# Performance work log

Measured on AMD Instinct MI355X. Metric: run time of the kernel, lower is better.

Reference implementation:

```python
import jax, jax.numpy as jnp
from jax import lax
import numpy as np

N, M, P, K = 2, 16384, 5023, 4
C_PLANE, HP = 32, 256
OUT_DIM = 32


def _harmonic(x):
    # pytorch3d HarmonicEmbedding(n=4, logspace, omega_0=1, append_input=True)
    f = jnp.asarray([1.0, 2.0, 4.0, 8.0], x.dtype)
    e = (x[..., None] * f).reshape(x.shape[:-1] + (-1,))  # [..., 12]
    return jnp.concatenate([jnp.sin(e), jnp.cos(e), x], axis=-1)  # [..., 27]


def _grid_sample2d(img, grid):
    # img [C,H,W], grid [M,2] (x->W, y->H) in [-1,1]; bilinear, zero pad, align_corners=False
    C, H, W = img.shape
    x = (grid[:, 0] + 1.0) * (W / 2.0) - 0.5
    y = (grid[:, 1] + 1.0) * (H / 2.0) - 0.5
    x0 = jnp.floor(x); y0 = jnp.floor(y)
    x1 = x0 + 1.0; y1 = y0 + 1.0
    wx1 = x - x0; wx0 = 1.0 - wx1
    wy1 = y - y0; wy0 = 1.0 - wy1
    def gather(ix, iy):
        valid = ((ix >= 0) & (ix < W) & (iy >= 0) & (iy < H)).astype(img.dtype)
        ixc = jnp.clip(ix, 0, W - 1).astype(jnp.int32)
        iyc = jnp.clip(iy, 0, H - 1).astype(jnp.int32)
        return img[:, iyc, ixc] * valid[None, :]  # [C,M]
    out = (gather(x0, y0) * (wx0 * wy0) + gather(x1, y0) * (wx1 * wy0)
           + gather(x0, y1) * (wx0 * wy1) + gather(x1, y1) * (wx1 * wy1))
    return out.T  # [M,C]


def _forward(coordinates, directions, points_position, tex_tplanes, emb_table,
             pw1, pb1, pw2, pb2, fw1, fb1, fw2, fb2, fw3, fb3, dw, db, rw1, rb1, rw2, rb2):
    c = coordinates
    p = points_position
    # --- triplane sampling (EG3D projections (x,y),(x,z),(z,x)), mean over planes ---
    proj = jnp.stack([c[..., :2],
                      c[..., jnp.array([0, 2])],
                      c[..., jnp.array([2, 0])]], axis=1)  # [N,3,M,2]
    tex = jax.vmap(jax.vmap(_grid_sample2d))(tex_tplanes, proj).mean(axis=1)  # [N,M,32]
    # --- KNN (squared distances, ascending, as pytorch3d knn_points) ---
    d2 = (jnp.sum(c * c, -1)[:, :, None] + jnp.sum(p * p, -1)[:, None, :]
          - 2.0 * jnp.einsum('nmc,npc->nmp', c, p))  # [N,M,P]
    negd, idx = lax.top_k(-d2, K)
    dist = -negd  # [N,M,K]
    nn = jax.vmap(lambda pts, i: pts[i])(p, idx)  # [N,M,K,3]
    pf = emb_table[idx]  # [N,M,K,32]
    rel = c[:, :, None, :] - nn
    rel = rel / jnp.maximum(jnp.linalg.norm(rel, axis=-1, keepdims=True), 1e-12)
    h = jnp.concatenate([pf, _harmonic(rel)], axis=-1)  # [N,M,K,59]
    h = jax.nn.relu(h @ pw1 + pb1) @ pw2 + pb2  # [N,M,K,32]
    w = 1.0 / dist
    w = w / jnp.sum(w, axis=1, keepdims=True)  # dim=1 exactly as in source
    pts_feat = jnp.sum(h * w[..., None], axis=2)  # [N,M,32]
    # --- dense MLP stack ---
    feat = jnp.concatenate([tex, pts_feat], axis=-1)  # [N,M,64]
    feat = jax.nn.relu(feat @ fw1 + fb1)
    feat = jax.nn.relu(feat @ fw2 + fb2)
    feat = feat @ fw3 + fb3  # [N,M,128]
    selector = jnp.all((c > -1.0) & (c < 1.0), axis=-1)  # [N,M]
    raw = (jax.nn.softplus(10.0 * (feat @ dw + db)) / 10.0) * selector[..., None]
    densities = 1.0 - jnp.exp(-raw)
    rays = directions / jnp.maximum(jnp.linalg.norm(directions, axis=-1, keepdims=True), 1e-12)
    rgb = jnp.concatenate([feat, _harmonic(rays)], axis=-1)  # [N,M,155]
    rgb = jax.nn.relu(rgb @ rw1 + rb1) @ rw2 + rb2  # [N,M,OUT_DIM]
    rgb = jnp.concatenate([jax.nn.sigmoid(rgb[..., :3]) * (1.0 + 2 * 0.001) - 0.001,
                           rgb[..., 3:]], axis=-1)
    return densities, rgb, dist


def setup_inputs() -> dict:
    key = jax.random.key(0)
    ks = jax.random.split(key, 16)
    rn = lambda k, s, sc=1.0: jax.random.normal(k, s, jnp.float32) * sc
    def lin(k, i, o):
        k1, k2 = jax.random.split(k)
        return rn(k1, (i, o), 1.0 / np.sqrt(i)), rn(k2, (o,), 0.01)
    coordinates = jax.random.uniform(ks[0], (N, M, 3), jnp.float32)
    directions = rn(ks[1], (N, M, 3))
    points_position = jax.random.uniform(ks[2], (N, P, 3), jnp.float32)
    tex_tplanes = rn(ks[3], (N, 3, C_PLANE, HP, HP))
    emb_table = rn(ks[4], (P, 32), 0.02)
    pw1, pb1 = lin(ks[5], 32 + 27, 64)
    pw2, pb2 = lin(ks[6], 64, 32)
    fw1, fb1 = lin(ks[7], 64, 128)
    fw2, fb2 = lin(ks[8], 128, 128)
    fw3, fb3 = lin(ks[9], 128, 128)
    dw, db = lin(ks[10], 128, 1)
    rw1, rb1 = lin(ks[11], 128 + 27, 64)
    rw2, rb2 = lin(ks[12], 64, OUT_DIM)
    return dict(coordinates=coordinates, directions=directions, points_position=points_position,
                tex_tplanes=tex_tplanes, emb_table=emb_table, pw1=pw1, pb1=pb1, pw2=pw2, pb2=pb2,
                fw1=fw1, fb1=fb1, fw2=fw2, fb2=fb2, fw3=fw3, fb3=fb3, dw=dw, db=db,
                rw1=rw1, rb1=rb1, rw2=rw2, rb2=rb2)


def reference(coordinates, directions, points_position, tex_tplanes, emb_table,
              pw1, pb1, pw2, pb2, fw1, fb1, fw2, fb2, fw3, fb3, dw, db, rw1, rb1, rw2, rb2):
    return _forward(coordinates, directions, points_position, tex_tplanes, emb_table,
                    pw1, pb1, pw2, pb2, fw1, fb1, fw2, fb2, fw3, fb3, dw, db, rw1, rb1, rw2, rb2)
```

## Files before the change

kernel.cpp:

```cpp
#include <hip/hip_runtime.h>
#include <float.h>
#include <math.h>

#define NB 2
#define MQ 16384
#define NQ (NB*MQ)
#define PP 5023
#define KNN 4
#define HPX 256
#define HWSZ (HPX*HPX)
#define GD 12
#define GC (GD*GD*GD)
#define CAND_MAX 1024

#define OUT_RGB_OFF  ((size_t)NQ)
#define OUT_DIST_OFF ((size_t)NQ + (size_t)NQ*32)

#define WS_SUMS_OFF   ((size_t)0x80000)
#define WS_PCNT_OFF   ((size_t)0x81000)
#define WS_PSTART_OFF ((size_t)0x85000)
#define WS_PCUR_OFF   ((size_t)0x89000)
#define WS_QCNT_OFF   ((size_t)0x8D000)
#define WS_QSTART_OFF ((size_t)0x91000)
#define WS_QCUR_OFF   ((size_t)0x95000)
// ... 168 lines not shown
    const int gz = c / (GD*GD), gy = (c / GD) % GD, gx = c % GD;

    const int x0 = max(gx-2,0), x1 = min(gx+2,GD-1);
    const int y0 = max(gy-2,0), y1 = min(gy+2,GD-1), ny = y1-y0+1;
    const int z0 = max(gz-2,0), z1 = min(gz+2,GD-1), nz = z1-z0+1;
    const int nrow = ny*nz;

    __shared__ unsigned int rcnt[25];
    if (tid < nrow) {
        const int yy = y0 + tid % ny;
        const int zz = z0 + tid / ny;
        const int c0 = n*GC + (zz*GD + yy)*GD + x0;
        const int c1 = n*GC + (zz*GD + yy)*GD + x1;
        const unsigned int s = pstart[c0];
        rs[tid]   = s;
        rcnt[tid] = (pstart[c1] + pcnt[c1]) - s;
    }
    __syncthreads();
    if (tid == 0) {
        unsigned int acc = 0; ro[0] = 0;
        for (int t = 0; t < nrow; ++t) { acc += rcnt[t]; ro[t+1] = acc; }
    }
    __syncthreads();
    const unsigned int total = ro[nrow];
    const bool ovf = (total > CAND_MAX);
    if (!ovf) {
        for (unsigned int i = tid; i < total; i += 256) {
            int lo = 0, hi = nrow;
            while (hi - lo > 1) { int mid = (lo + hi) >> 1; if (ro[mid] <= i) lo = mid; else hi = mid; }
            const unsigned int src = rs[lo] + (i - ro[lo]);
            cand[i] = pg[src];
            cidx[i] = pid[src];
        }
    }
    __syncthreads();

    const float w = 1.0f / (float)GD;
    const float thresh = 4.f * w * w * 0.999f;
    const int grp = tid >> 4, l16 = tid & 15;
    const unsigned int qs = qstart[n*GC + c];

#define INS4(d, i) { \
        bool L3 = ((d) < bd3) || ((d) == bd3 && (i) < bi3); \
        bool L2 = ((d) < bd2) || ((d) == bd2 && (i) < bi2); \
        bool L1 = ((d) < bd1) || ((d) == bd1 && (i) < bi1); \
        bool L0 = ((d) < bd0) || ((d) == bd0 && (i) < bi0); \
        bd3 = L3 ? (L2 ? bd2 : (d)) : bd3;  bi3 = L3 ? (L2 ? bi2 : (i)) : bi3; \
        bd2 = L2 ? (L1 ? bd1 : (d)) : bd2;  bi2 = L2 ? (L1 ? bi1 : (i)) : bi2; \
        bd1 = L1 ? (L0 ? bd0 : (d)) : bd1;  bi1 = L1 ? (L0 ? bi0 : (i)) : bi1; \
        bd0 = L0 ? (d) : bd0;               bi0 = L0 ? (i) : bi0; }

#define MERGE16() { \
        float bd[4] = { bd0, bd1, bd2, bd3 }; \
        int   bi[4] = { bi0, bi1, bi2, bi3 }; \
        for (int mask = 1; mask < 16; mask <<= 1) { \
            float od[4]; int oi[4]; \
            for (int j = 0; j < 4; ++j) { od[j] = __shfl_xor(bd[j], mask); \
                                          oi[j] = __shfl_xor(bi[j], mask); } \
            float e[4]; int ei[4]; \
            for (int j = 0; j < 4; ++j) { \
                float ad = bd[j], xd = od[3-j]; \
                int   ai = bi[j], xi = oi[3-j]; \
                bool ta = (ad < xd) || (ad == xd && ai < xi); \
                e[j] = ta ? ad : xd; ei[j] = ta ? ai : xi; \
            } \
            { bool sw = (e[2] < e[0]) || (e[2] == e[0] && ei[2] < ei[0]); \
              if (sw) { float td=e[0]; e[0]=e[2]; e[2]=td; int ti=ei[0]; ei[0]=ei[2]; ei[2]=ti; } } \
            { bool sw = (e[3] < e[1]) || (e[3] == e[1] && ei[3] < ei[1]); \
              if (sw) { float td=e[1]; e[1]=e[3]; e[3]=td; int ti=ei[1]; ei[1]=ei[3]; ei[3]=ti; } } \
            { bool sw = (e[1] < e[0]) || (e[1] == e[0] && ei[1] < ei[0]); \
              if (sw) { float td=e[0]; e[0]=e[1]; e[1]=td; int ti=ei[0]; ei[0]=ei[1]; ei[1]=ti; } } \
            { bool sw = (e[3] < e[2]) || (e[3] == e[2] && ei[3] < ei[2]); \
              if (sw) { float td=e[2]; e[2]=e[3]; e[3]=td; int ti=ei[2]; ei[2]=ei[3]; ei[3]=ti; } } \
            for (int j = 0; j < 4; ++j) { bd[j] = e[j]; bi[j] = ei[j]; } \
        } \
        bd0 = bd[0]; bd1 = bd[1]; bd2 = bd[2]; bd3 = bd[3]; \
        bi0 = bi[0]; bi1 = bi[1]; bi2 = bi[2]; bi3 = bi[3]; }

#pragma unroll 1
    for (unsigned int qb = 0; qb < qn; qb += 16) {
        const unsigned int qi = qb + grp;
        if (qi >= qn) continue;
        const int q = qid[qs + qi];
        const float cx = coords[3*q], cy = coords[3*q+1], cz = coords[3*q+2];
        const float ccq = fmaf(cx, cx, fmaf(cy, cy, cz*cz));

        float bd0 = FLT_MAX, bd1 = FLT_MAX, bd2 = FLT_MAX, bd3 = FLT_MAX;
        int   bi0 = 0x7fffffff, bi1 = 0x7fffffff, bi2 = 0x7fffffff, bi3 = 0x7fffffff;

        if (!ovf) {
#pragma unroll 1
            for (unsigned int j = l16; j < total; j += 16) {
                const float4 P = cand[j];
                const int i = cidx[j];
                const float dt = fmaf(cx, P.x, fmaf(cy, P.y, cz * P.z));
                const float d = fmaf(-2.0f, dt, ccq + P.w);
                INS4(d, i)
            }
            MERGE16()
        }
        if (ovf || !(bd3 < thresh)) {
            bd0 = bd1 = bd2 = bd3 = FLT_MAX;
            bi0 = bi1 = bi2 = bi3 = 0x7fffffff;
#pragma unroll 1
            for (int j = l16; j < PP; j += 16) {
                const float4 P = pg[n*PP + j];
                const int i = pid[n*PP + j];
                const float dt = fmaf(cx, P.x, fmaf(cy, P.y, cz * P.z));
                const float d = fmaf(-2.0f, dt, ccq + P.w);
                INS4(d, i)
            }
            MERGE16()
        }
        if (l16 == 0) {
            *(float4*)(odist + (size_t)q*4) = make_float4(bd0, bd1, bd2, bd3);
            *(int4*)(oidx + (size_t)q*4)    = make_int4(bi0, bi1, bi2, bi3);
        }
    }
#undef INS4
#undef MERGE16
}

__global__ __launch_bounds__(1024) void k_sums(const float* __restrict__ dist,
                                               float* __restrict__ sums) {
    const int b = blockIdx.x;
    const int n = b >> 2, k = b & 3;
    float s = 0.f;
    for (int m = threadIdx.x; m < MQ; m += 1024)
        s += 1.0f / dist[((size_t)n * MQ + m) * 4 + k];
    __shared__ float red[1024];
    red[threadIdx.x] = s;
    __syncthreads();
    for (int off = 512; off > 0; off >>= 1) {
        if (threadIdx.x < off) red[threadIdx.x] += red[threadIdx.x + off];
        __syncthreads();
    }
    if (threadIdx.x == 0) sums[b] = red[0];
}

static __device__ __forceinline__ float harm_val(int h, float rx, float ry, float rz) {
    if (h >= 27) return 0.f;
    float v;
    if (h < 24) {
        int base = (h < 12) ? h : (h - 12);
        float rv = (base >> 2) == 0 ? rx : ((base >> 2) == 1 ? ry : rz);
        float e = rv * (float)(1 << (base & 3));
        v = (h < 12) ? sinf(e) : cosf(e);
    } else {
        v = (h == 24) ? rx : ((h == 25) ? ry : rz);
    }
    return v;
}

#define SW 128

template<int DIN2, int DOUT, int TILE>
__device__ __forceinline__ void gemv2(const unsigned int* Xp, int lane,
                                      const unsigned int* Wl,
                                      const float* __restrict__ bias, int j0,
                                      float (&aa)[TILE], float (&ab)[TILE]) {
    static_assert(TILE % 4 == 0, "");
#pragma unroll
    for (int u = 0; u < TILE; ++u) { aa[u] = bias[j0 + u]; ab[u] = aa[u]; }
#pragma unroll
    for (int i2 = 0; i2 < DIN2; ++i2) {
        const uint2 xv = *(const uint2*)(Xp + i2 * SW + 2*lane);
        const uint4* wr = (const uint4*)(Wl + i2 * DOUT + j0);
#pragma unroll
        for (int t = 0; t < TILE/4; ++t) {
            const uint4 w4 = wr[t];
            aa[4*t+0] = dot2(xv.x, w4.x, aa[4*t+0]);  ab[4*t+0] = dot2(xv.y, w4.x, ab[4*t+0]);
            aa[4*t+1] = dot2(xv.x, w4.y, aa[4*t+1]);  ab[4*t+1] = dot2(xv.y, w4.y, ab[4*t+1]);
            aa[4*t+2] = dot2(xv.x, w4.z, aa[4*t+2]);  ab[4*t+2] = dot2(xv.y, w4.z, ab[4*t+2]);
            aa[4*t+3] = dot2(xv.x, w4.w, aa[4*t+3]);  ab[4*t+3] = dot2(xv.y, w4.w, ab[4*t+3]);
        }
    }
}

__global__ __launch_bounds__(1024, 1) void k_main(
    const float* __restrict__ coords, const float* __restrict__ dirs,
    const float* __restrict__ pts, const float* __restrict__ tex_raw,
    const unsigned int* __restrict__ tex16, const float* __restrict__ emb,
    const unsigned int* __restrict__ wp,
    const float* __restrict__ pb1, const float* __restrict__ pb2,
    const float* __restrict__ fb1, const float* __restrict__ fb2,
    const float* __restrict__ fb3, const float* __restrict__ db,
    const float* __restrict__ rb1, const float* __restrict__ rb2,
    const int* __restrict__ idxbuf, const float* __restrict__ distbuf,
    const float* __restrict__ sums, float* __restrict__ out, int use_tex_t)
{
    __shared__ unsigned int S[128 * SW];
    __shared__ __align__(16) unsigned int W[8192];
    const int tid  = threadIdx.x;
    const int lane = tid & 63;
    const int wv   = __builtin_amdgcn_readfirstlane(tid >> 6);
    const int q0   = blockIdx.x * 128;
    const int n    = q0 >> 14;
    const int qa   = q0 + 2*lane, qb = qa + 1;

#define STAGE(dstu4, srcoff, len) { \
        const uint4* s4_ = (const uint4*)(wp + (srcoff)); \
        for (int i_ = tid; i_ < (len)/4; i_ += 1024) ((uint4*)W)[(dstu4) + i_] = s4_[i_]; }

    unsigned int tex_pack[2];
    {
        const int g = wv;
#pragma unroll
        for (int s = 0; s < 2; ++s) {
            const int q = qa + s;
            const float cx = coords[q*3+0], cy = coords[q*3+1], cz = coords[q*3+2];
            float a0 = 0.f, a1 = 0.f;
#pragma unroll
            for (int pl = 0; pl < 3; ++pl) {
                float gx = (pl == 2) ? cz : cx;
                float gy = (pl == 0) ? cy : ((pl == 1) ? cz : cx);
                float x = (gx + 1.f) * 128.f - 0.5f;
                float y = (gy + 1.f) * 128.f - 0.5f;
                float x0f = floorf(x), y0f = floorf(y);
                float wx1 = x - x0f, wy1 = y - y0f;
                float wx0 = 1.f - wx1, wy0 = 1.f - wy1;
                int x0 = (int)x0f, y0 = (int)y0f;
                int n3 = n * 3 + pl;
                int  xs[4] = { x0, x0+1, x0,   x0+1 };
                int  ys[4] = { y0, y0,   y0+1, y0+1 };
                float wt[4] = { wx0*wy0, wx1*wy0, wx0*wy1, wx1*wy1 };
#pragma unroll
                for (int c = 0; c < 4; ++c) {
                    int xi = xs[c], yi = ys[c];
                    if (xi >= 0 && xi < HPX && yi >= 0 && yi < HPX) {
                        float wgt = wt[c];
                        if (use_tex_t) {
                            const unsigned int v = tex16[
                                ((size_t)n3 * HWSZ + (size_t)yi * HPX + xi) * 16 + g];
                            const float2 f = upk(v);
                            a0 = fmaf(wgt, f.x, a0);
                            a1 = fmaf(wgt, f.y, a1);
                        } else {
                            size_t base = ((size_t)(n3 * 32 + g * 2)) * HWSZ + (size_t)yi * HPX + xi;
                            a0 = fmaf(wgt, tex_raw[base], a0);
                            a1 = fmaf(wgt, tex_raw[base + HWSZ], a1);
                        }
                    }
                }
            }
            tex_pack[s] = pk2(a0 * (1.f/3.f), a1 * (1.f/3.f));
        }
    }

    STAGE(0, WP_PW1, 1920)
    STAGE(512, WP_PW2, 1024)
    __syncthreads();

#pragma unroll 1
    for (int k = 0; k < KNN; ++k) {
        {
#pragma unroll
            for (int s = 0; s < 2; ++s) {
                const int q = qa + s;
                const int id = idxbuf[(size_t)q*4 + k];
                if (wv < 8) {
                    const float4 e = *(const float4*)(emb + (size_t)id * 32 + wv*4);
                    S[(64 + 2*wv    )*SW + 2*lane + s] = pk2(e.x, e.y);
                    S[(64 + 2*wv + 1)*SW + 2*lane + s] = pk2(e.z, e.w);
                } else {
                    const int w8 = wv - 8;
                    if (w8 < 7) {
                        const float cx = coords[q*3+0], cy = coords[q*3+1], cz = coords[q*3+2];
                        const float nx = pts[((size_t)n*PP + id)*3 + 0];
                        const float ny = pts[((size_t)n*PP + id)*3 + 1];
                        const float nz = pts[((size_t)n*PP + id)*3 + 2];
                        float rx = cx - nx, ry = cy - ny, rz = cz - nz;
                        float nrm = sqrtf(fmaf(rx, rx, fmaf(ry, ry, rz*rz)));
                        float inv = 1.f / fmaxf(nrm, 1e-12f);
                        rx *= inv; ry *= inv; rz *= inv;
#pragma unroll
                        for (int t = 0; t < 2; ++t) {
                            const int pr = 2*w8 + t;
                            S[(80 + pr)*SW + 2*lane + s] =
                                pk2(harm_val(2*pr, rx, ry, rz), harm_val(2*pr + 1, rx, ry, rz));
                        }
                    }
                }
            }
        }
        __syncthreads();
        {
            float aa[4], ab[4];
            gemv2<30, 64, 4>(S + 64*SW, lane, W, pb1, wv * 4, aa, ab);
            S[(96 + 2*wv    )*SW + 2*lane + 0] = pk2(fmaxf(aa[0], 0.f), fmaxf(aa[1], 0.f));
            S[(96 + 2*wv    )*SW + 2*lane + 1] = pk2(fmaxf(ab[0], 0.f), fmaxf(ab[1], 0.f));
            S[(96 + 2*wv + 1)*SW + 2*lane + 0] = pk2(fmaxf(aa[2], 0.f), fmaxf(aa[3], 0.f));
            S[(96 + 2*wv + 1)*SW + 2*lane + 1] = pk2(fmaxf(ab[2], 0.f), fmaxf(ab[3], 0.f));
        }
        __syncthreads();
        {
            float aa[2], ab[2];
            aa[0] = pb2[wv*2 + 0]; aa[1] = pb2[wv*2 + 1];
            ab[0] = aa[0]; ab[1] = aa[1];
#pragma unroll
            for (int i2 = 0; i2 < 32; ++i2) {
                const uint2 xv = *(const uint2*)(S + (96 + i2)*SW + 2*lane);
                const unsigned int w0 = W[2048 + i2*32 + wv*2 + 0];
                const unsigned int w1 = W[2048 + i2*32 + wv*2 + 1];
                aa[0] = dot2(xv.x, w0, aa[0]);  ab[0] = dot2(xv.y, w0, ab[0]);
                aa[1] = dot2(xv.x, w1, aa[1]);  ab[1] = dot2(xv.y, w1, ab[1]);
            }
            const float da = distbuf[(size_t)qa*4 + k];
            const float dbq = distbuf[(size_t)qb*4 + k];
            const float wka = (1.0f / da)  / sums[n*4 + k];
            const float wkb = (1.0f / dbq) / sums[n*4 + k];
            S[(k*16 + wv)*SW + 2*lane + 0] = pk2(wka * aa[0], wka * aa[1]);
            S[(k*16 + wv)*SW + 2*lane + 1] = pk2(wkb * ab[0], wkb * ab[1]);
        }
        __syncthreads();
    }

    {
        S[(64 + wv)*SW + 2*lane + 0] = tex_pack[0];
        S[(64 + wv)*SW + 2*lane + 1] = tex_pack[1];
#pragma unroll
        for (int s = 0; s < 2; ++s) {
            float a = 0.f, b = 0.f;
#pragma unroll
            for (int k = 0; k < 4; ++k) {
                float2 v = upk(S[(k*16 + wv)*SW + 2*lane + s]);
                a += v.x; b += v.y;
            }
            S[(80 + wv)*SW + 2*lane + s] = pk2(a, b);
        }
    }
    STAGE(0, WP_FW1, 4096)
    __syncthreads();
    {
        float aa[8], ab[8];
        gemv2<32, 128, 8>(S + 64*SW, lane, W, fb1, wv * 8, aa, ab);
#pragma unroll
        for (int u = 0; u < 4; ++u) {
            S[(4*wv + u)*SW + 2*lane + 0] = pk2(fmaxf(aa[2*u], 0.f), fmaxf(aa[2*u+1], 0.f));
            S[(4*wv + u)*SW + 2*lane + 1] = pk2(fmaxf(ab[2*u], 0.f), fmaxf(ab[2*u+1], 0.f));
        }
    }
    __syncthreads();
    STAGE(0, WP_FW2, 8192)
    __syncthreads();
    {
        float aa[8], ab[8];
        gemv2<64, 128, 8>(S, lane, W, fb2, wv * 8, aa, ab);
#pragma unroll
        for (int u = 0; u < 4; ++u) {
            S[(64 + 4*wv + u)*SW + 2*lane + 0] = pk2(fmaxf(aa[2*u], 0.f), fmaxf(aa[2*u+1], 0.f));
            S[(64 + 4*wv + u)*SW + 2*lane + 1] = pk2(fmaxf(ab[2*u], 0.f), fmaxf(ab[2*u+1], 0.f));
        }
    }
    __syncthreads();
    STAGE(0, WP_FW3, 8192)
    __syncthreads();
    {
        float aa[8], ab[8];
        gemv2<64, 128, 8>(S + 64*SW, lane, W, fb3, wv * 8, aa, ab);
#pragma unroll
        for (int u = 0; u < 4; ++u) {
            S[(4*wv + u)*SW + 2*lane + 0] = pk2(aa[2*u], aa[2*u+1]);
            S[(4*wv + u)*SW + 2*lane + 1] = pk2(ab[2*u], ab[2*u+1]);
        }
    }
    __syncthreads();
    STAGE(0, WP_RW1, 4992)
    STAGE(1248, WP_RW2, 1024)
    STAGE(1504, WP_DW, 64)
    if (wv < 14) {
#pragma unroll
        for (int s = 0; s < 2; ++s) {
            const int q = qa + s;
            float dx = dirs[q*3+0], dy = dirs[q*3+1], dz = dirs[q*3+2];
            float dn = sqrtf(fmaf(dx, dx, fmaf(dy, dy, dz*dz)));
            float inv = 1.f / fmaxf(dn, 1e-12f);
            dx *= inv; dy *= inv; dz *= inv;
            S[(64 + wv)*SW + 2*lane + s] = pk2(harm_val(2*wv, dx, dy, dz),
                                               harm_val(2*wv + 1, dx, dy, dz));
        }
    }
    __syncthreads();
    {
        float aa[4], ab[4];
        gemv2<78, 64, 4>(S, lane, W, rb1, wv * 4, aa, ab);
        S[(78 + 2*wv    )*SW + 2*lane + 0] = pk2(fmaxf(aa[0], 0.f), fmaxf(aa[1], 0.f));
        S[(78 + 2*wv    )*SW + 2*lane + 1] = pk2(fmaxf(ab[0], 0.f), fmaxf(ab[1], 0.f));
        S[(78 + 2*wv + 1)*SW + 2*lane + 0] = pk2(fmaxf(aa[2], 0.f), fmaxf(aa[3], 0.f));
        S[(78 + 2*wv + 1)*SW + 2*lane + 1] = pk2(fmaxf(ab[2], 0.f), fmaxf(ab[3], 0.f));
    }
    __syncthreads();
    {
        float aa[2], ab[2];
        aa[0] = rb2[wv*2 + 0]; aa[1] = rb2[wv*2 + 1];
        ab[0] = aa[0]; ab[1] = aa[1];
#pragma unroll
        for (int i2 = 0; i2 < 32; ++i2) {
            const uint2 xv = *(const uint2*)(S + (78 + i2)*SW + 2*lane);
            const unsigned int w0 = W[4992 + i2*32 + wv*2 + 0];
            const unsigned int w1 = W[4992 + i2*32 + wv*2 + 1];
            aa[0] = dot2(xv.x, w0, aa[0]);  ab[0] = dot2(xv.y, w0, ab[0]);
            aa[1] = dot2(xv.x, w1, aa[1]);  ab[1] = dot2(xv.y, w1, ab[1]);
        }
#pragma unroll
        for (int u = 0; u < 2; ++u) {
            const int j = wv*2 + u;
            float va = (u == 0) ? aa[0] : aa[1];
            float vb = (u == 0) ? ab[0] : ab[1];
            if (j < 3) {
                va = 1.002f * (1.f / (1.f + expf(-va))) - 0.001f;
                vb = 1.002f * (1.f / (1.f + expf(-vb))) - 0.001f;
            }
            out[OUT_RGB_OFF + (size_t)qa*32 + j] = va;
            out[OUT_RGB_OFF + (size_t)qb*32 + j] = vb;
        }
        if (wv == 15) {
            float za = db[0], zb = db[0];
#pragma unroll 1
            for (int i2 = 0; i2 < 64; ++i2) {
                const uint2 xv = *(const uint2*)(S + i2*SW + 2*lane);
                const unsigned int wz = W[6016 + i2];
                za = dot2(xv.x, wz, za);
                zb = dot2(xv.y, wz, zb);
            }
#pragma unroll
            for (int s = 0; s < 2; ++s) {
                const int q = qa + s;
                const float z = (s == 0) ? za : zb;
                const float cx = coords[q*3+0], cy = coords[q*3+1], cz = coords[q*3+2];
                float selv = (cx > -1.f && cx < 1.f && cy > -1.f && cy < 1.f &&
                              cz > -1.f && cz < 1.f) ? 1.f : 0.f;
                float t10 = 10.f * z;
                float sp = (t10 > 20.f) ? t10 : log1pf(expf(t10));
                float raw = sp * 0.1f * selv;
                out[q] = 1.f - expf(-raw);
            }
        }
    }
#undef STAGE
}

extern "C" void kernel_launch(void* const* d_in, const int* in_sizes, int n_in,
                              void* d_out, int out_size, void* d_ws, size_t ws_size,
                              hipStream_t stream) {
    (void)in_sizes; (void)n_in; (void)out_size;
    const float* coords = (const float*)d_in[0];
    const float* dirs   = (const float*)d_in[1];
    const float* pts    = (const float*)d_in[2];
    const float* tex    = (const float*)d_in[3];
    const float* emb    = (const float*)d_in[4];
    const float* pw1 = (const float*)d_in[5];  const float* pb1 = (const float*)d_in[6];
    const float* pw2 = (const float*)d_in[7];  const float* pb2 = (const float*)d_in[8];
    const float* fw1 = (const float*)d_in[9];  const float* fb1 = (const float*)d_in[10];
    const float* fw2 = (const float*)d_in[11]; const float* fb2 = (const float*)d_in[12];
    const float* fw3 = (const float*)d_in[13]; const float* fb3 = (const float*)d_in[14];
    const float* dw  = (const float*)d_in[15]; const float* db  = (const float*)d_in[16];
    const float* rw1 = (const float*)d_in[17]; const float* rb1 = (const float*)d_in[18];
    const float* rw2 = (const float*)d_in[19]; const float* rb2 = (const float*)d_in[20];

    float*        out     = (float*)d_out;
    int*          wsidx   = (int*)d_ws;
    float*        wssums  = (float*)((char*)d_ws + WS_SUMS_OFF);
    unsigned int* wspcnt  = (unsigned int*)((char*)d_ws + WS_PCNT_OFF);
    unsigned int* wspsta  = (unsigned int*)((char*)d_ws + WS_PSTART_OFF);
    unsigned int* wspcur  = (unsigned int*)((char*)d_ws + WS_PCUR_OFF);
    unsigned int* wsqcnt  = (unsigned int*)((char*)d_ws + WS_QCNT_OFF);
    unsigned int* wsqsta  = (unsigned int*)((char*)d_ws + WS_QSTART_OFF);
    unsigned int* wsqcur  = (unsigned int*)((char*)d_ws + WS_QCUR_OFF);
    int*          wsqid   = (int*)((char*)d_ws + WS_QID_OFF);
    float4*       wspg    = (float4*)((char*)d_ws + WS_PG_OFF);
    int*          wspid   = (int*)((char*)d_ws + WS_PID_OFF);
    unsigned int* wswp    = (unsigned int*)((char*)d_ws + WS_WP_OFF);
    unsigned int* wstex   = (unsigned int*)((char*)d_ws + WS_TEX_OFF);

    const size_t need_tex = WS_TEX_OFF + (size_t)6 * HWSZ * 16 * 4;
    const int use_t = (ws_size >= need_tex) ? 1 : 0;

    PackArgs pa;
    pa.src[0] = pw1; pa.off[0] = WP_PW1; pa.din[0] = 59;  pa.dout[0] = 64;
    pa.src[1] = pw2; pa.off[1] = WP_PW2; pa.din[1] = 64;  pa.dout[1] = 32;
    pa.src[2] = fw1; pa.off[2] = WP_FW1; pa.din[2] = 64;  pa.dout[2] = 128;
    pa.src[3] = fw2; pa.off[3] = WP_FW2; pa.din[3] = 128; pa.dout[3] = 128;
    pa.src[4] = fw3; pa.off[4] = WP_FW3; pa.din[4] = 128; pa.dout[4] = 128;
    pa.src[5] = dw;  pa.off[5] = WP_DW;  pa.din[5] = 128; pa.dout[5] = 1;
    pa.src[6] = rw1; pa.off[6] = WP_RW1; pa.din[6] = 155; pa.dout[6] = 64;
    pa.src[7] = rw2; pa.off[7] = WP_RW2; pa.din[7] = 64;  pa.dout[7] = 32;

    const int nitems = NB*PP + NQ;
    hipMemsetAsync((char*)d_ws + WS_PCNT_OFF, 0, WS_QSTART_OFF - WS_PCNT_OFF, stream);
    k_pack<<<dim3(32, 8), 256, 0, stream>>>(pa, wswp);
    if (use_t) k_transpose<<<6 * 256, 256, 0, stream>>>(tex, wstex);
    k_count<<<(nitems + 255)/256, 256, 0, stream>>>(pts, coords, wspcnt, wsqcnt);
    k_scan2<<<1, 1024, 0, stream>>>(wspcnt, wspsta, wspcur, wsqcnt, wsqsta, wsqcur);
    k_scatter<<<(nitems + 255)/256, 256, 0, stream>>>(pts, coords, wspcur, wsqcur,
                                                      wspg, wspid, wsqid);
    k_knn_cell<<<NB*GC, 256, 0, stream>>>(coords, wspsta, wspcnt, wspg, wspid,
                                          wsqsta, wsqcnt, wsqid,
                                          out + OUT_DIST_OFF, wsidx);
    k_sums<<<8, 1024, 0, stream>>>(out + OUT_DIST_OFF, wssums);
    k_main<<<NQ / 128, 1024, 0, stream>>>(coords, dirs, pts, tex, wstex, emb,
                                          wswp, pb1, pb2, fb1, fb2, fb3, db, rb1, rb2,
                                          wsidx, out + OUT_DIST_OFF, wssums, out, use_t);
}
```

Baseline: 280.2 us.

## Process one query per lane in the main MLP kernel to raise occupancy

```diff
diff --git a/kernel.cpp b/kernel.cpp
--- a/kernel.cpp
+++ b/kernel.cpp
@@ -344,32 +344,32 @@
     return v;
 }
 
-#define SW 128
+#define SW 64
 
 template<int DIN2, int DOUT, int TILE>
-__device__ __forceinline__ void gemv2(const unsigned int* Xp, int lane,
+__device__ __forceinline__ void gemv1(const unsigned int* Xp, int lane,
                                       const unsigned int* Wl,
                                       const float* __restrict__ bias, int j0,
-                                      float (&aa)[TILE], float (&ab)[TILE]) {
+                                      float (&aa)[TILE]) {
     static_assert(TILE % 4 == 0, "");
 #pragma unroll
-    for (int u = 0; u < TILE; ++u) { aa[u] = bias[j0 + u]; ab[u] = aa[u]; }
+    for (int u = 0; u < TILE; ++u) aa[u] = bias[j0 + u];
 #pragma unroll
     for (int i2 = 0; i2 < DIN2; ++i2) {
-        const uint2 xv = *(const uint2*)(Xp + i2 * SW + 2*lane);
+        const unsigned int xv = Xp[i2 * SW + lane];
         const uint4* wr = (const uint4*)(Wl + i2 * DOUT + j0);
 #pragma unroll
         for (int t = 0; t < TILE/4; ++t) {
             const uint4 w4 = wr[t];
-            aa[4*t+0] = dot2(xv.x, w4.x, aa[4*t+0]);  ab[4*t+0] = dot2(xv.y, w4.x, ab[4*t+0]);
-            aa[4*t+1] = dot2(xv.x, w4.y, aa[4*t+1]);  ab[4*t+1] = dot2(xv.y, w4.y, ab[4*t+1]);
-            aa[4*t+2] = dot2(xv.x, w4.z, aa[4*t+2]);  ab[4*t+2] = dot2(xv.y, w4.z, ab[4*t+2]);
-            aa[4*t+3] = dot2(xv.x, w4.w, aa[4*t+3]);  ab[4*t+3] = dot2(xv.y, w4.w, ab[4*t+3]);
-        }
-    }
-}
-
-__global__ __launch_bounds__(1024, 1) void k_main(
+            aa[4*t+0] = dot2(xv, w4.x, aa[4*t+0]);
+            aa[4*t+1] = dot2(xv, w4.y, aa[4*t+1]);
+            aa[4*t+2] = dot2(xv, w4.z, aa[4*t+2]);
+            aa[4*t+3] = dot2(xv, w4.w, aa[4*t+3]);
+        }
+    }
+}
+
+__global__ __launch_bounds__(1024, 8) void k_main(
     const float* __restrict__ coords, const float* __restrict__ dirs,
     const float* __restrict__ pts, const float* __restrict__ tex_raw,
     const unsigned int* __restrict__ tex16, const float* __restrict__ emb,
@@ -386,57 +386,54 @@
     const int tid  = threadIdx.x;
     const int lane = tid & 63;
     const int wv   = __builtin_amdgcn_readfirstlane(tid >> 6);
-    const int q0   = blockIdx.x * 128;
+    const int q0   = blockIdx.x * 64;
     const int n    = q0 >> 14;
-    const int qa   = q0 + 2*lane, qb = qa + 1;
+    const int qa   = q0 + lane;
 
 #define STAGE(dstu4, srcoff, len) { \
         const uint4* s4_ = (const uint4*)(wp + (srcoff)); \
         for (int i_ = tid; i_ < (len)/4; i_ += 1024) ((uint4*)W)[(dstu4) + i_] = s4_[i_]; }
 
-    unsigned int tex_pack[2];
+    unsigned int tex_pack;
     {
         const int g = wv;
-#pragma unroll
-        for (int s = 0; s < 2; ++s) {
-            const int q = qa + s;
-            const float cx = coords[q*3+0], cy = coords[q*3+1], cz = coords[q*3+2];
-            float a0 = 0.f, a1 = 0.f;
-#pragma unroll
-            for (int pl = 0; pl < 3; ++pl) {
-                float gx = (pl == 2) ? cz : cx;
-                float gy = (pl == 0) ? cy : ((pl == 1) ? cz : cx);
-                float x = (gx + 1.f) * 128.f - 0.5f;
-                float y = (gy + 1.f) * 128.f - 0.5f;
-                float x0f = floorf(x), y0f = floorf(y);
-                float wx1 = x - x0f, wy1 = y - y0f;
-                float wx0 = 1.f - wx1, wy0 = 1.f - wy1;
-                int x0 = (int)x0f, y0 = (int)y0f;
-                int n3 = n * 3 + pl;
-                int  xs[4] = { x0, x0+1, x0,   x0+1 };
-                int  ys[4] = { y0, y0,   y0+1, y0+1 };
-                float wt[4] = { wx0*wy0, wx1*wy0, wx0*wy1, wx1*wy1 };
-#pragma unroll
-                for (int c = 0; c < 4; ++c) {
-                    int xi = xs[c], yi = ys[c];
-                    if (xi >= 0 && xi < HPX && yi >= 0 && yi < HPX) {
-                        float wgt = wt[c];
-                        if (use_tex_t) {
-                            const unsigned int v = tex16[
-                                ((size_t)n3 * HWSZ + (size_t)yi * HPX + xi) * 16 + g];
-                            const float2 f = upk(v);
-                            a0 = fmaf(wgt, f.x, a0);
-                            a1 = fmaf(wgt, f.y, a1);
-                        } else {
-                            size_t base = ((size_t)(n3 * 32 + g * 2)) * HWSZ + (size_t)yi * HPX + xi;
-                            a0 = fmaf(wgt, tex_raw[base], a0);
-                            a1 = fmaf(wgt, tex_raw[base + HWSZ], a1);
-                        }
+        const int q = qa;
+        const float cx = coords[q*3+0], cy = coords[q*3+1], cz = coords[q*3+2];
+        float a0 = 0.f, a1 = 0.f;
+#pragma unroll
+        for (int pl = 0; pl < 3; ++pl) {
+            float gx = (pl == 2) ? cz : cx;
+            float gy = (pl == 0) ? cy : ((pl == 1) ? cz : cx);
+            float x = (gx + 1.f) * 128.f - 0.5f;
+            float y = (gy + 1.f) * 128.f - 0.5f;
+            float x0f = floorf(x), y0f = floorf(y);
+            float wx1 = x - x0f, wy1 = y - y0f;
+            float wx0 = 1.f - wx1, wy0 = 1.f - wy1;
+            int x0 = (int)x0f, y0 = (int)y0f;
+            int n3 = n * 3 + pl;
+            int  xs[4] = { x0, x0+1, x0,   x0+1 };
+            int  ys[4] = { y0, y0,   y0+1, y0+1 };
+            float wt[4] = { wx0*wy0, wx1*wy0, wx0*wy1, wx1*wy1 };
+#pragma unroll
+            for (int c = 0; c < 4; ++c) {
+                int xi = xs[c], yi = ys[c];
+                if (xi >= 0 && xi < HPX && yi >= 0 && yi < HPX) {
+                    float wgt = wt[c];
+                    if (use_tex_t) {
+                        const unsigned int v = tex16[
+                            ((size_t)n3 * HWSZ + (size_t)yi * HPX + xi) * 16 + g];
+                        const float2 f = upk(v);
+                        a0 = fmaf(wgt, f.x, a0);
+                        a1 = fmaf(wgt, f.y, a1);
+                    } else {
+                        size_t base = ((size_t)(n3 * 32 + g * 2)) * HWSZ + (size_t)yi * HPX + xi;
+                        a0 = fmaf(wgt, tex_raw[base], a0);
+                        a1 = fmaf(wgt, tex_raw[base + HWSZ], a1);
                     }
                 }
             }
-            tex_pack[s] = pk2(a0 * (1.f/3.f), a1 * (1.f/3.f));
-        }
+        }
+        tex_pack = pk2(a0 * (1.f/3.f), a1 * (1.f/3.f));
     }
 
     STAGE(0, WP_PW1, 1920)
@@ -446,187 +443,154 @@
 #pragma unroll 1
     for (int k = 0; k < KNN; ++k) {
         {
-#pragma unroll
-            for (int s = 0; s < 2; ++s) {
-                const int q = qa + s;
-                const int id = idxbuf[(size_t)q*4 + k];
-                if (wv < 8) {
-                    const float4 e = *(const float4*)(emb + (size_t)id * 32 + wv*4);
-                    S[(64 + 2*wv    )*SW + 2*lane + s] = pk2(e.x, e.y);
-                    S[(64 + 2*wv + 1)*SW + 2*lane + s] = pk2(e.z, e.w);
-                } else {
-                    const int w8 = wv - 8;
-                    if (w8 < 7) {
-                        const float cx = coords[q*3+0], cy = coords[q*3+1], cz = coords[q*3+2];
-                        const float nx = pts[((size_t)n*PP + id)*3 + 0];
-                        const float ny = pts[((size_t)n*PP + id)*3 + 1];
-                        const float nz = pts[((size_t)n*PP + id)*3 + 2];
-                        float rx = cx - nx, ry = cy - ny, rz = cz - nz;
-                        float nrm = sqrtf(fmaf(rx, rx, fmaf(ry, ry, rz*rz)));
-                        float inv = 1.f / fmaxf(nrm, 1e-12f);
-                        rx *= inv; ry *= inv; rz *= inv;
-#pragma unroll
-                        for (int t = 0; t < 2; ++t) {
-                            const int pr = 2*w8 + t;
-                            S[(80 + pr)*SW + 2*lane + s] =
-                                pk2(harm_val(2*pr, rx, ry, rz), harm_val(2*pr + 1, rx, ry, rz));
-                        }
+            const int q = qa;
+            const int id = idxbuf[(size_t)q*4 + k];
+            if (wv < 8) {
+                const float4 e = *(const float4*)(emb + (size_t)id * 32 + wv*4);
+                S[(64 + 2*wv    )*SW + lane] = pk2(e.x, e.y);
+                S[(64 + 2*wv + 1)*SW + lane] = pk2(e.z, e.w);
+            } else {
+                const int w8 = wv - 8;
+                if (w8 < 7) {
+                    const float cx = coords[q*3+0], cy = coords[q*3+1], cz = coords[q*3+2];
+                    const float nx = pts[((size_t)n*PP + id)*3 + 0];
+                    const float ny = pts[((size_t)n*PP + id)*3 + 1];
+                    const float nz = pts[((size_t)n*PP + id)*3 + 2];
+                    float rx = cx - nx, ry = cy - ny, rz = cz - nz;
+                    float nrm = sqrtf(fmaf(rx, rx, fmaf(ry, ry, rz*rz)));
+                    float inv = 1.f / fmaxf(nrm, 1e-12f);
+                    rx *= inv; ry *= inv; rz *= inv;
+#pragma unroll
+                    for (int t = 0; t < 2; ++t) {
+                        const int pr = 2*w8 + t;
+                        S[(80 + pr)*SW + lane] =
+                            pk2(harm_val(2*pr, rx, ry, rz), harm_val(2*pr + 1, rx, ry, rz));
                     }
                 }
             }
         }
         __syncthreads();
         {
-            float aa[4], ab[4];
-            gemv2<30, 64, 4>(S + 64*SW, lane, W, pb1, wv * 4, aa, ab);
-            S[(96 + 2*wv    )*SW + 2*lane + 0] = pk2(fmaxf(aa[0], 0.f), fmaxf(aa[1], 0.f));
-            S[(96 + 2*wv    )*SW + 2*lane + 1] = pk2(fmaxf(ab[0], 0.f), fmaxf(ab[1], 0.f));
-            S[(96 + 2*wv + 1)*SW + 2*lane + 0] = pk2(fmaxf(aa[2], 0.f), fmaxf(aa[3], 0.f));
-            S[(96 + 2*wv + 1)*SW + 2*lane + 1] = pk2(fmaxf(ab[2], 0.f), fmaxf(ab[3], 0.f));
+            float aa[4];
+            gemv1<30, 64, 4>(S + 64*SW, lane, W, pb1, wv * 4, aa);
+            S[(96 + 2*wv    )*SW + lane] = pk2(fmaxf(aa[0], 0.f), fmaxf(aa[1], 0.f));
+            S[(96 + 2*wv + 1)*SW + lane] = pk2(fmaxf(aa[2], 0.f), fmaxf(aa[3], 0.f));
         }
         __syncthreads();
         {
-            float aa[2], ab[2];
+            float aa[2];
             aa[0] = pb2[wv*2 + 0]; aa[1] = pb2[wv*2 + 1];
-            ab[0] = aa[0]; ab[1] = aa[1];
 #pragma unroll
             for (int i2 = 0; i2 < 32; ++i2) {
-                const uint2 xv = *(const uint2*)(S + (96 + i2)*SW + 2*lane);
+                const unsigned int xv = S[(96 + i2)*SW + lane];
                 const unsigned int w0 = W[2048 + i2*32 + wv*2 + 0];
                 const unsigned int w1 = W[2048 + i2*32 + wv*2 + 1];
-                aa[0] = dot2(xv.x, w0, aa[0]);  ab[0] = dot2(xv.y, w0, ab[0]);
-                aa[1] = dot2(xv.x, w1, aa[1]);  ab[1] = dot2(xv.y, w1, ab[1]);
+                aa[0] = dot2(xv, w0, aa[0]);
+                aa[1] = dot2(xv, w1, aa[1]);
             }
             const float da = distbuf[(size_t)qa*4 + k];
-            const float dbq = distbuf[(size_t)qb*4 + k];
-            const float wka = (1.0f / da)  / sums[n*4 + k];
-            const float wkb = (1.0f / dbq) / sums[n*4 + k];
-            S[(k*16 + wv)*SW + 2*lane + 0] = pk2(wka * aa[0], wka * aa[1]);
-            S[(k*16 + wv)*SW + 2*lane + 1] = pk2(wkb * ab[0], wkb * ab[1]);
+            const float wka = (1.0f / da) / sums[n*4 + k];
+            S[(k*16 + wv)*SW + lane] = pk2(wka * aa[0], wka * aa[1]);
         }
         __syncthreads();
     }
 
     {
-        S[(64 + wv)*SW + 2*lane + 0] = tex_pack[0];
-        S[(64 + wv)*SW + 2*lane + 1] = tex_pack[1];
-#pragma unroll
-        for (int s = 0; s < 2; ++s) {
-            float a = 0.f, b = 0.f;
-#pragma unroll
-            for (int k = 0; k < 4; ++k) {
-                float2 v = upk(S[(k*16 + wv)*SW + 2*lane + s]);
-                a += v.x; b += v.y;
-            }
-            S[(80 + wv)*SW + 2*lane + s] = pk2(a, b);
-        }
+        S[(64 + wv)*SW + lane] = tex_pack;
+        float a = 0.f, b = 0.f;
+#pragma unroll
+        for (int k = 0; k < 4; ++k) {
+            float2 v = upk(S[(k*16 + wv)*SW + lane]);
+            a += v.x; b += v.y;
+        }
+        S[(80 + wv)*SW + lane] = pk2(a, b);
     }
     STAGE(0, WP_FW1, 4096)
     __syncthreads();
     {
-        float aa[8], ab[8];
-        gemv2<32, 128, 8>(S + 64*SW, lane, W, fb1, wv * 8, aa, ab);
-#pragma unroll
-        for (int u = 0; u < 4; ++u) {
-            S[(4*wv + u)*SW + 2*lane + 0] = pk2(fmaxf(aa[2*u], 0.f), fmaxf(aa[2*u+1], 0.f));
-            S[(4*wv + u)*SW + 2*lane + 1] = pk2(fmaxf(ab[2*u], 0.f), fmaxf(ab[2*u+1], 0.f));
-        }
+        float aa[8];
+        gemv1<32, 128, 8>(S + 64*SW, lane, W, fb1, wv * 8, aa);
+#pragma unroll
+        for (int u = 0; u < 4; ++u)
+            S[(4*wv + u)*SW + lane] = pk2(fmaxf(aa[2*u], 0.f), fmaxf(aa[2*u+1], 0.f));
     }
     __syncthreads();
     STAGE(0, WP_FW2, 8192)
     __syncthreads();
     {
-        float aa[8], ab[8];
-        gemv2<64, 128, 8>(S, lane, W, fb2, wv * 8, aa, ab);
-#pragma unroll
-        for (int u = 0; u < 4; ++u) {
-            S[(64 + 4*wv + u)*SW + 2*lane + 0] = pk2(fmaxf(aa[2*u], 0.f), fmaxf(aa[2*u+1], 0.f));
-            S[(64 + 4*wv + u)*SW + 2*lane + 1] = pk2(fmaxf(ab[2*u], 0.f), fmaxf(ab[2*u+1], 0.f));
-        }
+        float aa[8];
+        gemv1<64, 128, 8>(S, lane, W, fb2, wv * 8, aa);
+#pragma unroll
+        for (int u = 0; u < 4; ++u)
+            S[(64 + 4*wv + u)*SW + lane] = pk2(fmaxf(aa[2*u], 0.f), fmaxf(aa[2*u+1], 0.f));
     }
     __syncthreads();
     STAGE(0, WP_FW3, 8192)
     __syncthreads();
     {
-        float aa[8], ab[8];
-        gemv2<64, 128, 8>(S + 64*SW, lane, W, fb3, wv * 8, aa, ab);
-#pragma unroll
-        for (int u = 0; u < 4; ++u) {
-            S[(4*wv + u)*SW + 2*lane + 0] = pk2(aa[2*u], aa[2*u+1]);
-            S[(4*wv + u)*SW + 2*lane + 1] = pk2(ab[2*u], ab[2*u+1]);
-        }
+        float aa[8];
+        gemv1<64, 128, 8>(S + 64*SW, lane, W, fb3, wv * 8, aa);
+#pragma unroll
+        for (int u = 0; u < 4; ++u)
+            S[(4*wv + u)*SW + lane] = pk2(aa[2*u], aa[2*u+1]);
     }
     __syncthreads();
     STAGE(0, WP_RW1, 4992)
     STAGE(1248, WP_RW2, 1024)
     STAGE(1504, WP_DW, 64)
     if (wv < 14) {
-#pragma unroll
-        for (int s = 0; s < 2; ++s) {
-            const int q = qa + s;
-            float dx = dirs[q*3+0], dy = dirs[q*3+1], dz = dirs[q*3+2];
-            float dn = sqrtf(fmaf(dx, dx, fmaf(dy, dy, dz*dz)));
-            float inv = 1.f / fmaxf(dn, 1e-12f);
-            dx *= inv; dy *= inv; dz *= inv;
-            S[(64 + wv)*SW + 2*lane + s] = pk2(harm_val(2*wv, dx, dy, dz),
-                                               harm_val(2*wv + 1, dx, dy, dz));
-        }
+        const int q = qa;
+        float dx = dirs[q*3+0], dy = dirs[q*3+1], dz = dirs[q*3+2];
+        float dn = sqrtf(fmaf(dx, dx, fmaf(dy, dy, dz*dz)));
+        float inv = 1.f / fmaxf(dn, 1e-12f);
+        dx *= inv; dy *= inv; dz *= inv;
+        S[(64 + wv)*SW + lane] = pk2(harm_val(2*wv, dx, dy, dz),
+                                     harm_val(2*wv + 1, dx, dy, dz));
     }
     __syncthreads();
     {
-        float aa[4], ab[4];
-        gemv2<78, 64, 4>(S, lane, W, rb1, wv * 4, aa, ab);
-        S[(78 + 2*wv    )*SW + 2*lane + 0] = pk2(fmaxf(aa[0], 0.f), fmaxf(aa[1], 0.f));
-        S[(78 + 2*wv    )*SW + 2*lane + 1] = pk2(fmaxf(ab[0], 0.f), fmaxf(ab[1], 0.f));
-        S[(78 + 2*wv + 1)*SW + 2*lane + 0] = pk2(fmaxf(aa[2], 0.f), fmaxf(aa[3], 0.f));
-        S[(78 + 2*wv + 1)*SW + 2*lane + 1] = pk2(fmaxf(ab[2], 0.f), fmaxf(ab[3], 0.f));
+        float aa[4];
+        gemv1<78, 64, 4>(S, lane, W, rb1, wv * 4, aa);
+        S[(78 + 2*wv    )*SW + lane] = pk2(fmaxf(aa[0], 0.f), fmaxf(aa[1], 0.f));
+        S[(78 + 2*wv + 1)*SW + lane] = pk2(fmaxf(aa[2], 0.f), fmaxf(aa[3], 0.f));
     }
     __syncthreads();
     {
-        float aa[2], ab[2];
+        float aa[2];
         aa[0] = rb2[wv*2 + 0]; aa[1] = rb2[wv*2 + 1];
-        ab[0] = aa[0]; ab[1] = aa[1];
 #pragma unroll
         for (int i2 = 0; i2 < 32; ++i2) {
-            const uint2 xv = *(const uint2*)(S + (78 + i2)*SW + 2*lane);
+            const unsigned int xv = S[(78 + i2)*SW + lane];
             const unsigned int w0 = W[4992 + i2*32 + wv*2 + 0];
             const unsigned int w1 = W[4992 + i2*32 + wv*2 + 1];
-            aa[0] = dot2(xv.x, w0, aa[0]);  ab[0] = dot2(xv.y, w0, ab[0]);
-            aa[1] = dot2(xv.x, w1, aa[1]);  ab[1] = dot2(xv.y, w1, ab[1]);
+            aa[0] = dot2(xv, w0, aa[0]);
+            aa[1] = dot2(xv, w1, aa[1]);
         }
 #pragma unroll
         for (int u = 0; u < 2; ++u) {
             const int j = wv*2 + u;
-            float va = (u == 0) ? aa[0] : aa[1];
-            float vb = (u == 0) ? ab[0] : ab[1];
+            float va = aa[u];
             if (j < 3) {
                 va = 1.002f * (1.f / (1.f + expf(-va))) - 0.001f;
-                vb = 1.002f * (1.f / (1.f + expf(-vb))) - 0.001f;
             }
             out[OUT_RGB_OFF + (size_t)qa*32 + j] = va;
-            out[OUT_RGB_OFF + (size_t)qb*32 + j] = vb;
         }
         if (wv == 15) {
-            float za = db[0], zb = db[0];
+            float za = db[0];
 #pragma unroll 1
             for (int i2 = 0; i2 < 64; ++i2) {
-                const uint2 xv = *(const uint2*)(S + i2*SW + 2*lane);
+                const unsigned int xv = S[i2*SW + lane];
                 const unsigned int wz = W[6016 + i2];
-                za = dot2(xv.x, wz, za);
-                zb = dot2(xv.y, wz, zb);
-            }
-#pragma unroll
-            for (int s = 0; s < 2; ++s) {
-                const int q = qa + s;
-                const float z = (s == 0) ? za : zb;
-                const float cx = coords[q*3+0], cy = coords[q*3+1], cz = coords[q*3+2];
-                float selv = (cx > -1.f && cx < 1.f && cy > -1.f && cy < 1.f &&
-                              cz > -1.f && cz < 1.f) ? 1.f : 0.f;
-                float t10 = 10.f * z;
-                float sp = (t10 > 20.f) ? t10 : log1pf(expf(t10));
-                float raw = sp * 0.1f * selv;
-                out[q] = 1.f - expf(-raw);
-            }
+                za = dot2(xv, wz, za);
+            }
+            const int q = qa;
+            const float cx = coords[q*3+0], cy = coords[q*3+1], cz = coords[q*3+2];
+            float selv = (cx > -1.f && cx < 1.f && cy > -1.f && cy < 1.f &&
+                          cz > -1.f && cz < 1.f) ? 1.f : 0.f;
+            float t10 = 10.f * za;
+            float sp = (t10 > 20.f) ? t10 : log1pf(expf(t10));
+            float raw = sp * 0.1f * selv;
+            out[q] = 1.f - expf(-raw);
         }
     }
 #undef STAGE
@@ -690,7 +654,7 @@
                                           wsqsta, wsqcnt, wsqid,
                                           out + OUT_DIST_OFF, wsidx);
     k_sums<<<8, 1024, 0, stream>>>(out + OUT_DIST_OFF, wssums);
-    k_main<<<NQ / 128, 1024, 0, stream>>>(coords, dirs, pts, tex, wstex, emb,
-                                          wswp, pb1, pb2, fb1, fb2, fb3, db, rb1, rb2,
-                                          wsidx, out + OUT_DIST_OFF, wssums, out, use_t);
-}
+    k_main<<<NQ / 64, 1024, 0, stream>>>(coords, dirs, pts, tex, wstex, emb,
+                                         wswp, pb1, pb2, fb1, fb2, fb3, db, rb1, rb2,
+                                         wsidx, out + OUT_DIST_OFF, wssums, out, use_t);
+}
```

Result: slower. 307.4 us (+9.7%).

## Read MLP weights from global memory and coalesce RGB output stores via LDS

Applied to the files above, without the earlier changes.

```diff
diff --git a/kernel.cpp b/kernel.cpp
--- a/kernel.cpp
+++ b/kernel.cpp
@@ -348,7 +348,7 @@
 
 template<int DIN2, int DOUT, int TILE>
 __device__ __forceinline__ void gemv2(const unsigned int* Xp, int lane,
-                                      const unsigned int* Wl,
+                                      const unsigned int* __restrict__ Wg,
                                       const float* __restrict__ bias, int j0,
                                       float (&aa)[TILE], float (&ab)[TILE]) {
     static_assert(TILE % 4 == 0, "");
@@ -357,7 +357,7 @@
 #pragma unroll
     for (int i2 = 0; i2 < DIN2; ++i2) {
         const uint2 xv = *(const uint2*)(Xp + i2 * SW + 2*lane);
-        const uint4* wr = (const uint4*)(Wl + i2 * DOUT + j0);
+        const uint4* wr = (const uint4*)(Wg + i2 * DOUT + j0);
 #pragma unroll
         for (int t = 0; t < TILE/4; ++t) {
             const uint4 w4 = wr[t];
@@ -382,17 +382,13 @@
     const float* __restrict__ sums, float* __restrict__ out, int use_tex_t)
 {
     __shared__ unsigned int S[128 * SW];
-    __shared__ __align__(16) unsigned int W[8192];
+    __shared__ float Rstg[128 * 33];
     const int tid  = threadIdx.x;
     const int lane = tid & 63;
     const int wv   = __builtin_amdgcn_readfirstlane(tid >> 6);
     const int q0   = blockIdx.x * 128;
     const int n    = q0 >> 14;
     const int qa   = q0 + 2*lane, qb = qa + 1;
-
-#define STAGE(dstu4, srcoff, len) { \
-        const uint4* s4_ = (const uint4*)(wp + (srcoff)); \
-        for (int i_ = tid; i_ < (len)/4; i_ += 1024) ((uint4*)W)[(dstu4) + i_] = s4_[i_]; }
 
     unsigned int tex_pack[2];
     {
@@ -438,10 +434,6 @@
             tex_pack[s] = pk2(a0 * (1.f/3.f), a1 * (1.f/3.f));
         }
     }
-
-    STAGE(0, WP_PW1, 1920)
-    STAGE(512, WP_PW2, 1024)
-    __syncthreads();
 
 #pragma unroll 1
     for (int k = 0; k < KNN; ++k) {
@@ -478,7 +470,7 @@
         __syncthreads();
         {
             float aa[4], ab[4];
-            gemv2<30, 64, 4>(S + 64*SW, lane, W, pb1, wv * 4, aa, ab);
+            gemv2<30, 64, 4>(S + 64*SW, lane, wp + WP_PW1, pb1, wv * 4, aa, ab);
             S[(96 + 2*wv    )*SW + 2*lane + 0] = pk2(fmaxf(aa[0], 0.f), fmaxf(aa[1], 0.f));
             S[(96 + 2*wv    )*SW + 2*lane + 1] = pk2(fmaxf(ab[0], 0.f), fmaxf(ab[1], 0.f));
             S[(96 + 2*wv + 1)*SW + 2*lane + 0] = pk2(fmaxf(aa[2], 0.f), fmaxf(aa[3], 0.f));
@@ -486,16 +478,16 @@
         }
         __syncthreads();
         {
+            const unsigned int* __restrict__ pw2g = wp + WP_PW2;
             float aa[2], ab[2];
             aa[0] = pb2[wv*2 + 0]; aa[1] = pb2[wv*2 + 1];
             ab[0] = aa[0]; ab[1] = aa[1];
 #pragma unroll
             for (int i2 = 0; i2 < 32; ++i2) {
                 const uint2 xv = *(const uint2*)(S + (96 + i2)*SW + 2*lane);
-                const unsigned int w0 = W[2048 + i2*32 + wv*2 + 0];
-                const unsigned int w1 = W[2048 + i2*32 + wv*2 + 1];
-                aa[0] = dot2(xv.x, w0, aa[0]);  ab[0] = dot2(xv.y, w0, ab[0]);
-                aa[1] = dot2(xv.x, w1, aa[1]);  ab[1] = dot2(xv.y, w1, ab[1]);
+                const uint2 wv2 = *(const uint2*)(pw2g + i2*32 + wv*2);
+                aa[0] = dot2(xv.x, wv2.x, aa[0]);  ab[0] = dot2(xv.y, wv2.x, ab[0]);
+                aa[1] = dot2(xv.x, wv2.y, aa[1]);  ab[1] = dot2(xv.y, wv2.y, ab[1]);
             }
             const float da = distbuf[(size_t)qa*4 + k];
             const float dbq = distbuf[(size_t)qb*4 + k];
@@ -521,11 +513,10 @@
             S[(80 + wv)*SW + 2*lane + s] = pk2(a, b);
         }
     }
-    STAGE(0, WP_FW1, 4096)
     __syncthreads();
     {
         float aa[8], ab[8];
-        gemv2<32, 128, 8>(S + 64*SW, lane, W, fb1, wv * 8, aa, ab);
+        gemv2<32, 128, 8>(S + 64*SW, lane, wp + WP_FW1, fb1, wv * 8, aa, ab);
 #pragma unroll
         for (int u = 0; u < 4; ++u) {
             S[(4*wv + u)*SW + 2*lane + 0] = pk2(fmaxf(aa[2*u], 0.f), fmaxf(aa[2*u+1], 0.f));
@@ -533,11 +524,9 @@
         }
     }
     __syncthreads();
-    STAGE(0, WP_FW2, 8192)
-    __syncthreads();
     {
         float aa[8], ab[8];
-        gemv2<64, 128, 8>(S, lane, W, fb2, wv * 8, aa, ab);
+        gemv2<64, 128, 8>(S, lane, wp + WP_FW2, fb2, wv * 8, aa, ab);
 #pragma unroll
         for (int u = 0; u < 4; ++u) {
             S[(64 + 4*wv + u)*SW + 2*lane + 0] = pk2(fmaxf(aa[2*u], 0.f), fmaxf(aa[2*u+1], 0.f));
@@ -545,11 +534,9 @@
         }
     }
     __syncthreads();
-    STAGE(0, WP_FW3, 8192)
-    __syncthreads();
     {
         float aa[8], ab[8];
-        gemv2<64, 128, 8>(S + 64*SW, lane, W, fb3, wv * 8, aa, ab);
+        gemv2<64, 128, 8>(S + 64*SW, lane, wp + WP_FW3, fb3, wv * 8, aa, ab);
 #pragma unroll
         for (int u = 0; u < 4; ++u) {
             S[(4*wv + u)*SW + 2*lane + 0] = pk2(aa[2*u], aa[2*u+1]);
@@ -557,9 +544,6 @@
         }
     }
     __syncthreads();
-    STAGE(0, WP_RW1, 4992)
-    STAGE(1248, WP_RW2, 1024)
-    STAGE(1504, WP_DW, 64)
     if (wv < 14) {
 #pragma unroll
         for (int s = 0; s < 2; ++s) {
@@ -575,7 +559,7 @@
     __syncthreads();
     {
         float aa[4], ab[4];
-        gemv2<78, 64, 4>(S, lane, W, rb1, wv * 4, aa, ab);
+        gemv2<78, 64, 4>(S, lane, wp + WP_RW1, rb1, wv * 4, aa, ab);
         S[(78 + 2*wv    )*SW + 2*lane + 0] = pk2(fmaxf(aa[0], 0.f), fmaxf(aa[1], 0.f));
         S[(78 + 2*wv    )*SW + 2*lane + 1] = pk2(fmaxf(ab[0], 0.f), fmaxf(ab[1], 0.f));
         S[(78 + 2*wv + 1)*SW + 2*lane + 0] = pk2(fmaxf(aa[2], 0.f), fmaxf(aa[3], 0.f));
@@ -583,16 +567,16 @@
     }
     __syncthreads();
     {
+        const unsigned int* __restrict__ rw2g = wp + WP_RW2;
         float aa[2], ab[2];
         aa[0] = rb2[wv*2 + 0]; aa[1] = rb2[wv*2 + 1];
         ab[0] = aa[0]; ab[1] = aa[1];
 #pragma unroll
         for (int i2 = 0; i2 < 32; ++i2) {
             const uint2 xv = *(const uint2*)(S + (78 + i2)*SW + 2*lane);
-            const unsigned int w0 = W[4992 + i2*32 + wv*2 + 0];
-            const unsigned int w1 = W[4992 + i2*32 + wv*2 + 1];
-            aa[0] = dot2(xv.x, w0, aa[0]);  ab[0] = dot2(xv.y, w0, ab[0]);
-            aa[1] = dot2(xv.x, w1, aa[1]);  ab[1] = dot2(xv.y, w1, ab[1]);
+            const uint2 wv2 = *(const uint2*)(rw2g + i2*32 + wv*2);
+            aa[0] = dot2(xv.x, wv2.x, aa[0]);  ab[0] = dot2(xv.y, wv2.x, ab[0]);
+            aa[1] = dot2(xv.x, wv2.y, aa[1]);  ab[1] = dot2(xv.y, wv2.y, ab[1]);
         }
 #pragma unroll
         for (int u = 0; u < 2; ++u) {
@@ -603,15 +587,16 @@
                 va = 1.002f * (1.f / (1.f + expf(-va))) - 0.001f;
                 vb = 1.002f * (1.f / (1.f + expf(-vb))) - 0.001f;
             }
-            out[OUT_RGB_OFF + (size_t)qa*32 + j] = va;
-            out[OUT_RGB_OFF + (size_t)qb*32 + j] = vb;
+            Rstg[(2*lane    ) * 33 + j] = va;
+            Rstg[(2*lane + 1) * 33 + j] = vb;
         }
         if (wv == 15) {
+            const unsigned int* __restrict__ dwg = wp + WP_DW;
             float za = db[0], zb = db[0];
-#pragma unroll 1
+#pragma unroll 8
             for (int i2 = 0; i2 < 64; ++i2) {
                 const uint2 xv = *(const uint2*)(S + i2*SW + 2*lane);
-                const unsigned int wz = W[6016 + i2];
+                const unsigned int wz = dwg[i2];
                 za = dot2(xv.x, wz, za);
                 zb = dot2(xv.y, wz, zb);
             }
@@ -629,7 +614,17 @@
             }
         }
     }
-#undef STAGE
+    __syncthreads();
+    {
+        const int cq = tid >> 3;
+        const int j0 = (tid & 7) * 4;
+        float4 v;
+        v.x = Rstg[cq*33 + j0 + 0];
+        v.y = Rstg[cq*33 + j0 + 1];
+        v.z = Rstg[cq*33 + j0 + 2];
+        v.w = Rstg[cq*33 + j0 + 3];
+        *(float4*)(out + OUT_RGB_OFF + ((size_t)(q0 + cq))*32 + j0) = v;
+    }
 }
 
 extern "C" void kernel_launch(void* const* d_in, const int* in_sizes, int n_in,
```

New measurement: 302.2 us. 1.08x slower.
